# Optimization experiments

Hardware: AMD Instinct MI355X
Metric: run time of the kernel (lower is better)

The kernel has to match this reference:

```python
import jax, jax.numpy as jnp
import numpy as np

# Irreps spec: 32x0e (dim 1, with bias) + 16x1o (dim 3) + 8x2e (dim 5)
# x: [B, n_channels_in, 120] where 120 = 32*1 + 16*3 + 8*5

B = 1024
N_IN = 256
N_OUT = 256


def setup_inputs() -> dict:
    key = jax.random.key(0)
    k_x, k0, k1, k2 = jax.random.split(key, 4)
    std = 1.0 / np.sqrt(N_IN)
    x = jax.random.normal(k_x, (B, N_IN, 120), dtype=jnp.float32)
    W0 = jax.random.normal(k0, (32, N_OUT, N_IN), dtype=jnp.float32) * std
    W1 = jax.random.normal(k1, (16, N_OUT, N_IN), dtype=jnp.float32) * std
    W2 = jax.random.normal(k2, (8, N_OUT, N_IN), dtype=jnp.float32) * std
    b0 = jnp.zeros((32, N_OUT), dtype=jnp.float32)
    return {"x": x, "W0": W0, "W1": W1, "W2": W2, "b0": b0}


def reference(x, W0, W1, W2, b0):
    # Grouped form of the original per-multiplicity loop. Slices of the last
    # axis are consecutive per (irrep, multiplicity), so reshaping a group of
    # `mul` copies of an irrep of dim `d` to [..., n_in, mul, d] and doing one
    # batched einsum reproduces the original concatenation order exactly.
    groups = [(W0, 1, b0), (W1, 3, None), (W2, 5, None)]  # (weights[mul,o,i], irrep dim, bias[mul,o] or None)
    outs = []
    start = 0
    for W, d, b in groups:
        mul = W.shape[0]
        width = mul * d
        xs = x[..., start:start + width].reshape(*x.shape[:-1], mul, d)  # [..., n_in, mul, d]
        y = jnp.einsum('moi,...imd->...omd', W, xs)  # [..., n_out, mul, d]
        if b is not None:  # only l=0 irreps get a bias, broadcast over d (=1)
            y = y + b.T[:, :, None]  # [n_out, mul, 1]
        outs.append(y.reshape(*y.shape[:-2], width))  # [..., n_out, mul*d]
        start += width
    return jnp.concatenate(outs, axis=-1)  # [..., n_out, 120]
```

## Files before the change

kernel.cpp:

```cpp
#include <hip/hip_runtime.h>

typedef __attribute__((ext_vector_type(8))) short bf16x8;
typedef __attribute__((ext_vector_type(4))) float f32x4;
typedef __attribute__((ext_vector_type(8))) unsigned short u16x8;

#define DEVINL __device__ __forceinline__
#define AS1 __attribute__((address_space(1)))
#define AS3 __attribute__((address_space(3)))

constexpr int NI = 256;
constexpr int NO = 256;
constexpr int NC = 120;
constexpr int WELEMS = 56 * NO * NI;
constexpr size_t XT_ELEMS = (size_t)NC * 1024 * NI;

DEVINL ushort f2bf(float x) {
  unsigned u = __float_as_uint(x);
  u += 0x7FFFu + ((u >> 16) & 1u);
  return (ushort)(u >> 16);
}
DEVINL float bf2f(ushort v) { return __uint_as_float((unsigned)v << 16); }

__global__ __launch_bounds__(256) void prep_w(const float* __restrict__ w0,
                                              const float* __restrict__ w1,
                                              const float* __restrict__ w2,
                                              ushort* __restrict__ wb) {
  const int m = blockIdx.x >> 5;
  const int kc = blockIdx.x & 31;
  const int o = threadIdx.x;
  const float* src;
  if (m < 32)      src = w0 + ((size_t)(m * NO + o)) * NI;
  else if (m < 48) src = w1 + ((size_t)((m - 32) * NO + o)) * NI;
  else             src = w2 + ((size_t)((m - 48) * NO + o)) * NI;
  src += kc * 8;
  float4 a = *reinterpret_cast<const float4*>(src);
  float4 b = *reinterpret_cast<const float4*>(src + 4);
  u16x8 p = { f2bf(a.x), f2bf(a.y), f2bf(a.z), f2bf(a.w),
              f2bf(b.x), f2bf(b.y), f2bf(b.z), f2bf(b.w) };
  *reinterpret_cast<u16x8*>(wb + ((size_t)(blockIdx.x * 256 + o)) * 8) = p;
}

__global__ __launch_bounds__(256) void xpose(const float* __restrict__ x,
                                             ushort* __restrict__ xt) {
  __shared__ ushort tl[120 * 128];
  const int bid = blockIdx.x;
  const int b = bid >> 1, ih = bid & 1;
  const int t = threadIdx.x;
  const float* xb = x + (size_t)b * (NI * NC) + (size_t)ih * 128 * NC;
#pragma unroll
  for (int j = 0; j < 15; ++j) {
    const int e = j * 1024 + t * 4;
    f32x4 v = *reinterpret_cast<const f32x4*>(xb + e);
    const int i = e / 120, c = e % 120;
#pragma unroll
    for (int k = 0; k < 4; ++k)
      tl[(c + k) * 128 + (i ^ ((((c + k) >> 2) & 31) << 2))] = f2bf(v[k]);
  }
  __syncthreads();
  ushort* dst = xt + (size_t)b * NI + ih * 128;
#pragma unroll
  for (int q = 0; q < 15; ++q) {
    const int chunk = q * 256 + t;
    const int c = chunk >> 5, i0 = (chunk & 31) * 4;
    ushort4 v = *reinterpret_cast<const ushort4*>(
        &tl[c * 128 + (i0 ^ (((c >> 2) & 31) << 2))]);
    *reinterpret_cast<ushort4*>(dst + (size_t)c * (1024 * NI) + i0) = v;
  }
}

__global__ __launch_bounds__(256, 4) void e3mix6(ushort* xt,
                                                 const ushort* __restrict__ wb,
                                                 const float* __restrict__ bias0) {
  __shared__ ushort xs[2][64 * 64];
  const int bid = blockIdx.x;
  const int c  = bid % 120;
  const int bt = bid / 120;
  const int m  = c < 32 ? c : (c < 80 ? 32 + (c - 32) / 3 : 48 + (c - 80) / 5);
  const int bg = bt * 64;

  const int tid = threadIdx.x, lane = tid & 63, wid = tid >> 6;
  const int rb = lane & 15, rg = lane >> 4;
  const int wo = wid * 64;

  const int srow = wid * 16 + (lane >> 3);
  const ushort* gsrc = xt + (size_t)c * (1024 * NI) + (size_t)(bg + srow) * NI
                          + ((lane & 7) ^ (srow & 7)) * 8;
  ushort* ldst0 = &xs[0][wid * 1024];
  ushort* ldst1 = &xs[1][wid * 1024];

  f32x4 acc[4][4];
#pragma unroll
  for (int i = 0; i < 4; ++i)
#pragma unroll
    for (int j = 0; j < 4; ++j) acc[i][j] = (f32x4)0.0f;

#define STAGE(LD, S)                                                          \
  do {                                                                        \
    __builtin_amdgcn_global_load_lds((const AS1 void*)(gsrc + (S) * 64),      \
                                     (AS3 void*)(LD), 16, 0, 0);              \
    __builtin_amdgcn_global_load_lds((const AS1 void*)(gsrc + (S) * 64 + 8 * NI), \
                                     (AS3 void*)((LD) + 512), 16, 0, 0);      \
  } while (0)

  STAGE(ldst0, 0);
  __syncthreads();

#pragma unroll 1
  for (int s = 0; s < 4; ++s) {
    if (s < 3) STAGE((s & 1) ? ldst0 : ldst1, s + 1);
    const ushort* xb = xs[s & 1];
#pragma unroll
    for (int kh = 0; kh < 2; ++kh) {
      bf16x8 a[4], w[4];
#pragma unroll
      for (int fb = 0; fb < 4; ++fb)
        a[fb] = *reinterpret_cast<const bf16x8*>(
            &xb[(fb * 16 + rb) * 64 + (((kh * 4 + rg) ^ (rb & 7)) * 8)]);
#pragma unroll
      for (int fo = 0; fo < 4; ++fo)
        w[fo] = *reinterpret_cast<const bf16x8*>(
            wb + ((size_t)((m * 32 + s * 8 + kh * 4 + rg) * NO
                           + wo + fo * 16 + rb)) * 8);
#pragma unroll
      for (int fb = 0; fb < 4; ++fb)
#pragma unroll
        for (int fo = 0; fo < 4; ++fo)
          acc[fb][fo] = __builtin_amdgcn_mfma_f32_16x16x32_bf16(a[fb], w[fo],
                                                                acc[fb][fo], 0, 0, 0);
    }
    __syncthreads();
  }
#undef STAGE

  if (c < 32) {
#pragma unroll
    for (int fo = 0; fo < 4; ++fo) {
      const float bv = bias0[c * NO + wo + fo * 16 + rb];
#pragma unroll
      for (int fb = 0; fb < 4; ++fb) acc[fb][fo] += bv;
    }
  }

  ushort* ot = xt + (size_t)c * (1024 * NI);
#pragma unroll
  for (int fb = 0; fb < 4; ++fb)
#pragma unroll
    for (int r = 0; r < 4; ++r) {
      const size_t brow = (size_t)(bg + fb * 16 + rg * 4 + r) * NO;
#pragma unroll
      for (int fo = 0; fo < 4; ++fo)
        ot[brow + wo + fo * 16 + rb] = f2bf(acc[fb][fo][r]);
    }
}

__global__ __launch_bounds__(256) void otrans(const ushort* __restrict__ xt,
                                              float* __restrict__ out) {
  __shared__ ushort tl[120 * 132];
  const int bid = blockIdx.x;
  const int b = bid >> 1, oh = bid & 1;
  const int t = threadIdx.x;
  const ushort* src = xt + (size_t)b * NO + oh * 128;
#pragma unroll
  for (int q = 0; q < 15; ++q) {
    const int chunk = q * 256 + t;
    const int c = chunk >> 5, i0 = (chunk & 31) * 4;
    ushort4 v = *reinterpret_cast<const ushort4*>(
        src + (size_t)c * (1024 * NI) + i0);
    *reinterpret_cast<ushort4*>(&tl[c * 132 + i0]) = v;
  }
  __syncthreads();
  const int op = t & 127, ch = t >> 7;
  float* dst = out + ((size_t)b * NO + oh * 128 + op) * NC + ch * 60;
#pragma unroll
  for (int j = 0; j < 15; ++j) {
    float4 v;
    v.x = bf2f(tl[(ch * 60 + 4 * j + 0) * 132 + op]);
    v.y = bf2f(tl[(ch * 60 + 4 * j + 1) * 132 + op]);
    v.z = bf2f(tl[(ch * 60 + 4 * j + 2) * 132 + op]);
    v.w = bf2f(tl[(ch * 60 + 4 * j + 3) * 132 + op]);
    *reinterpret_cast<float4*>(dst + 4 * j) = v;
  }
}

__global__ __launch_bounds__(512, 4) void e3mix2f(const float* __restrict__ x,
                                                  const ushort* __restrict__ wb,
                                                  const float* __restrict__ bias0,
                                                  float* __restrict__ out) {
  __shared__ ushort xs[8 * 16 * 64];
  const int bid = blockIdx.x;
  const int ct = bid % 15, bt = bid / 15;
  const int c0 = ct * 8, bg = bt * 16;
  const int t = threadIdx.x, lane = t & 63, wid = t >> 6;
  const int sb = lane >> 2, sp = lane & 3;
  const int rb = lane & 15, rg = lane >> 4;
  const int oc = wid * 16 + rb;
  const int srow = (wid * 16 + sb) * 64;
  const int sk0 = (sp * 16) ^ ((sb & 7) << 3);
  const int sk1 = (sp * 16 + 8) ^ ((sb & 7) << 3);

  f32x4 acc[8][2];
#pragma unroll
  for (int i = 0; i < 8; ++i) { acc[i][0] = (f32x4)0.0f; acc[i][1] = (f32x4)0.0f; }
  bf16x8 w00 = {}, w01 = {}, w10 = {}, w11 = {};

#pragma unroll 1
  for (int s = 0; s < 4; ++s) {
    if (s) __syncthreads();
    u16x8 v0, v1;
    const float* src = x + (size_t)(bg + sb) * (NI * NC)
                         + (size_t)(s * 64 + sp * 16) * NC + (c0 + wid);
#pragma unroll
    for (int jj = 0; jj < 8; ++jj) v0[jj] = f2bf(src[jj * NC]);
#pragma unroll
    for (int jj = 0; jj < 8; ++jj) v1[jj] = f2bf(src[(8 + jj) * NC]);
    *reinterpret_cast<u16x8*>(&xs[srow + sk0]) = v0;
    *reinterpret_cast<u16x8*>(&xs[srow + sk1]) = v1;
    __syncthreads();

    int mprev = -1;
#pragma unroll
    for (int cc = 0; cc < 8; ++cc) {
      const int c = c0 + cc;
      const int m = c < 32 ? c : (c < 80 ? 32 + (c - 32) / 3 : 48 + (c - 80) / 5);
      if (m != mprev) {
        const ushort* wp = wb + ((size_t)((m * 32 + s * 8 + rg) * NO + oc)) * 8;
        w00 = *reinterpret_cast<const bf16x8*>(wp);
        w10 = *reinterpret_cast<const bf16x8*>(wp + (size_t)4 * NO * 8);
        w01 = *reinterpret_cast<const bf16x8*>(wp + 128 * 8);
        w11 = *reinterpret_cast<const bf16x8*>(wp + (size_t)4 * NO * 8 + 128 * 8);
        mprev = m;
      }
      const ushort* xp = xs + (cc * 16 + rb) * 64;
      const int sz = (rb & 7) << 3;
      bf16x8 a0 = *reinterpret_cast<const bf16x8*>(xp + ((rg * 8) ^ sz));
      bf16x8 a1 = *reinterpret_cast<const bf16x8*>(xp + ((32 + rg * 8) ^ sz));
      acc[cc][0] = __builtin_amdgcn_mfma_f32_16x16x32_bf16(a0, w00, acc[cc][0], 0, 0, 0);
      acc[cc][0] = __builtin_amdgcn_mfma_f32_16x16x32_bf16(a1, w10, acc[cc][0], 0, 0, 0);
      acc[cc][1] = __builtin_amdgcn_mfma_f32_16x16x32_bf16(a0, w01, acc[cc][1], 0, 0, 0);
      acc[cc][1] = __builtin_amdgcn_mfma_f32_16x16x32_bf16(a1, w11, acc[cc][1], 0, 0, 0);
    }
  }

  if (c0 < 32) {
#pragma unroll
    for (int cc = 0; cc < 8; ++cc) {
      acc[cc][0] += bias0[(c0 + cc) * NO + oc];
      acc[cc][1] += bias0[(c0 + cc) * NO + oc + 128];
    }
  }

  const int br0 = bg + rg * 4;
#pragma unroll
  for (int of = 0; of < 2; ++of)
#pragma unroll
    for (int r = 0; r < 4; ++r) {
      float4 va = make_float4(acc[0][of][r], acc[1][of][r], acc[2][of][r], acc[3][of][r]);
      float4 vb = make_float4(acc[4][of][r], acc[5][of][r], acc[6][of][r], acc[7][of][r]);
      float* dst = out + ((size_t)(br0 + r) * NO + oc + of * 128) * NC + c0;
      *reinterpret_cast<float4*>(dst) = va;
      *reinterpret_cast<float4*>(dst + 4) = vb;
    }
}

extern "C" void kernel_launch(void* const* d_in, const int* in_sizes, int n_in,
                              void* d_out, int out_size, void* d_ws, size_t ws_size,
                              hipStream_t stream) {
  const float* x  = (const float*)d_in[0];
  const float* w0 = (const float*)d_in[1];
  const float* w1 = (const float*)d_in[2];
  const float* w2 = (const float*)d_in[3];
  const float* b0 = (const float*)d_in[4];
  float* out = (float*)d_out;
  ushort* wb = (ushort*)d_ws;
  ushort* xt = wb + WELEMS;

  prep_w<<<56 * 32, 256, 0, stream>>>(w0, w1, w2, wb);
  const bool big = ws_size >= (size_t)2 * (WELEMS + XT_ELEMS);
  if (big) {
    xpose<<<2048, 256, 0, stream>>>(x, xt);
    e3mix6<<<16 * 120, 256, 0, stream>>>(xt, wb, b0);
    otrans<<<2048, 256, 0, stream>>>(xt, out);
  } else {
    e3mix2f<<<960, 512, 0, stream>>>(x, wb, b0, out);
  }
}
```

Baseline: 136.8 us.

## Store intermediate bf16 buffer batch-major to localize transpose writes

Changes the intermediate xt layout from channel-major [c][b][i] to batch-major [b][c][i], so each transpose block writes one contiguous batch row and otrans reads contiguous memory. The xpose kernel now stages fp32 in padded LDS over quarter-blocks of inputs (4096 blocks) and converts to bf16 on the way out. The GEMM kernel's loads and stores are readdressed with the BROW stride, which spreads each block's rows across a larger stride and may hurt locality for the MFMA stage.

```diff
diff --git a/kernel.cpp b/kernel.cpp
--- a/kernel.cpp
+++ b/kernel.cpp
@@ -11,6 +11,7 @@
 constexpr int NI = 256;
 constexpr int NO = 256;
 constexpr int NC = 120;
+constexpr int BROW = NC * NI;
 constexpr int WELEMS = 56 * NO * NI;
 constexpr size_t XT_ELEMS = (size_t)NC * 1024 * NI;
 
@@ -42,33 +43,35 @@
 
 __global__ __launch_bounds__(256) void xpose(const float* __restrict__ x,
                                              ushort* __restrict__ xt) {
-  __shared__ ushort tl[120 * 128];
-  const int bid = blockIdx.x;
-  const int b = bid >> 1, ih = bid & 1;
+  __shared__ float tl[64 * 121];
+  const int bid = blockIdx.x;
+  const int b = bid >> 2, iq = bid & 3;
   const int t = threadIdx.x;
-  const float* xb = x + (size_t)b * (NI * NC) + (size_t)ih * 128 * NC;
+  const float* xb = x + (size_t)b * BROW + (size_t)iq * 64 * NC;
 #pragma unroll
   for (int j = 0; j < 15; ++j) {
-    const int e = j * 1024 + t * 4;
-    f32x4 v = *reinterpret_cast<const f32x4*>(xb + e);
+    const int e = (j * 256 + t) * 2;
+    float2 v = *reinterpret_cast<const float2*>(xb + e);
     const int i = e / 120, c = e % 120;
-#pragma unroll
-    for (int k = 0; k < 4; ++k)
-      tl[(c + k) * 128 + (i ^ ((((c + k) >> 2) & 31) << 2))] = f2bf(v[k]);
+    tl[i * 121 + c] = v.x;
+    tl[i * 121 + c + 1] = v.y;
   }
   __syncthreads();
-  ushort* dst = xt + (size_t)b * NI + ih * 128;
-#pragma unroll
-  for (int q = 0; q < 15; ++q) {
+  ushort* dst = xt + (size_t)b * BROW + iq * 64;
+#pragma unroll
+  for (int q = 0; q < 4; ++q) {
     const int chunk = q * 256 + t;
-    const int c = chunk >> 5, i0 = (chunk & 31) * 4;
-    ushort4 v = *reinterpret_cast<const ushort4*>(
-        &tl[c * 128 + (i0 ^ (((c >> 2) & 31) << 2))]);
-    *reinterpret_cast<ushort4*>(dst + (size_t)c * (1024 * NI) + i0) = v;
-  }
-}
-
-__global__ __launch_bounds__(256, 4) void e3mix6(ushort* xt,
+    if (chunk < 960) {
+      const int c = chunk >> 3, ich = chunk & 7;
+      u16x8 p;
+#pragma unroll
+      for (int k = 0; k < 8; ++k) p[k] = f2bf(tl[(ich * 8 + k) * 121 + c]);
+      *reinterpret_cast<u16x8*>(dst + (size_t)c * NI + ich * 8) = p;
+    }
+  }
+}
+
+__global__ __launch_bounds__(256, 4) void e3mix7(ushort* xt,
                                                  const ushort* __restrict__ wb,
                                                  const float* __restrict__ bias0) {
   __shared__ ushort xs[2][64 * 64];
@@ -83,7 +86,7 @@
   const int wo = wid * 64;
 
   const int srow = wid * 16 + (lane >> 3);
-  const ushort* gsrc = xt + (size_t)c * (1024 * NI) + (size_t)(bg + srow) * NI
+  const ushort* gsrc = xt + (size_t)(bg + srow) * BROW + (size_t)c * NI
                           + ((lane & 7) ^ (srow & 7)) * 8;
   ushort* ldst0 = &xs[0][wid * 1024];
   ushort* ldst1 = &xs[1][wid * 1024];
@@ -98,7 +101,8 @@
   do {                                                                        \
     __builtin_amdgcn_global_load_lds((const AS1 void*)(gsrc + (S) * 64),      \
                                      (AS3 void*)(LD), 16, 0, 0);              \
-    __builtin_amdgcn_global_load_lds((const AS1 void*)(gsrc + (S) * 64 + 8 * NI), \
+    __builtin_amdgcn_global_load_lds((const AS1 void*)(gsrc + (S) * 64        \
+                                                       + (size_t)8 * BROW),   \
                                      (AS3 void*)((LD) + 512), 16, 0, 0);      \
   } while (0)
 
@@ -141,15 +145,14 @@
     }
   }
 
-  ushort* ot = xt + (size_t)c * (1024 * NI);
 #pragma unroll
   for (int fb = 0; fb < 4; ++fb)
 #pragma unroll
     for (int r = 0; r < 4; ++r) {
-      const size_t brow = (size_t)(bg + fb * 16 + rg * 4 + r) * NO;
+      ushort* ot = xt + (size_t)(bg + fb * 16 + rg * 4 + r) * BROW + (size_t)c * NI;
 #pragma unroll
       for (int fo = 0; fo < 4; ++fo)
-        ot[brow + wo + fo * 16 + rb] = f2bf(acc[fb][fo][r]);
+        ot[wo + fo * 16 + rb] = f2bf(acc[fb][fo][r]);
     }
 }
 
@@ -159,14 +162,13 @@
   const int bid = blockIdx.x;
   const int b = bid >> 1, oh = bid & 1;
   const int t = threadIdx.x;
-  const ushort* src = xt + (size_t)b * NO + oh * 128;
+  const ushort* src = xt + (size_t)b * BROW + oh * 128;
 #pragma unroll
   for (int q = 0; q < 15; ++q) {
     const int chunk = q * 256 + t;
-    const int c = chunk >> 5, i0 = (chunk & 31) * 4;
-    ushort4 v = *reinterpret_cast<const ushort4*>(
-        src + (size_t)c * (1024 * NI) + i0);
-    *reinterpret_cast<ushort4*>(&tl[c * 132 + i0]) = v;
+    const int c = chunk >> 5, o4 = (chunk & 31) * 4;
+    ushort4 v = *reinterpret_cast<const ushort4*>(src + (size_t)c * NI + o4);
+    *reinterpret_cast<ushort4*>(&tl[c * 132 + o4]) = v;
   }
   __syncthreads();
   const int op = t & 127, ch = t >> 7;
@@ -277,8 +279,8 @@
   prep_w<<<56 * 32, 256, 0, stream>>>(w0, w1, w2, wb);
   const bool big = ws_size >= (size_t)2 * (WELEMS + XT_ELEMS);
   if (big) {
-    xpose<<<2048, 256, 0, stream>>>(x, xt);
-    e3mix6<<<16 * 120, 256, 0, stream>>>(xt, wb, b0);
+    xpose<<<4096, 256, 0, stream>>>(x, xt);
+    e3mix7<<<16 * 120, 256, 0, stream>>>(xt, wb, b0);
     otrans<<<2048, 256, 0, stream>>>(xt, out);
   } else {
     e3mix2f<<<960, 512, 0, stream>>>(x, wb, b0, out);
```

Measured after the change: 132.2 us. 3.3% less time.
